# Kernel optimization log

Measured on AMD Instinct MI355X. Metric: run time of the kernel, lower is better.

Reference implementation:

```python
import jax, jax.numpy as jnp
import numpy as np

B, N, M, D, BD = 4, 128, 128, 256, 1024


def setup_inputs() -> dict:
    key = jax.random.key(0)
    k1, k2, k3, k4 = jax.random.split(key, 4)
    stdv = 1.0 / np.sqrt(D)
    X = jax.random.normal(k1, (B, N, D), dtype=jnp.float32)
    Y = jax.random.normal(k2, (B, M, D), dtype=jnp.float32)
    # bilinear tensor, init uniform(-stdv, stdv) as in reset_parameters
    A = jax.random.uniform(k3, (D, D, BD), minval=-stdv, maxval=stdv, dtype=jnp.float32)
    # final Linear(bd, 1)
    W = jax.random.uniform(k4, (1, BD), minval=-1.0 / np.sqrt(BD), maxval=1.0 / np.sqrt(BD), dtype=jnp.float32)
    b = jnp.zeros((1,), dtype=jnp.float32)
    return {"X": X, "Y": Y, "A": A, "W": W, "b": b}


def reference(X, Y, A, W, b):
    # Fused version of the per-slice loop: bi[b,n,m,k] = X[b,n,:] @ A[:,:,k] @ Y[b,m,:]
    # Step 1: contract X with A over d -> [B, N, d, bd]
    t = jnp.einsum('bnd,dek->bnek', X, A)
    # Step 2: contract with Y over the second feature dim -> [B, N, M, bd]
    bi = jnp.einsum('bnek,bme->bnmk', t, Y)
    # fc: single Linear(bd, 1), no trailing ReLU (fc_lst[:-1] drops it)
    S = jnp.einsum('bnmk,ok->bnmo', bi, W) + b
    return S[..., 0]  # squeeze to [B, N, M]
```

## Files before the change

kernel.cpp:

```cpp
#include <hip/hip_runtime.h>

#define DD   256
#define BD   1024
#define NB   4
#define NN   128
#define MM   128

__global__ __launch_bounds__(256) void reduce_A_kernel(
    const float* __restrict__ A, const float* __restrict__ W,
    float* __restrict__ Aw)
{
    __shared__ float wsh[BD];
    const int t = threadIdx.x;
#pragma unroll
    for (int i = 0; i < 4; ++i) wsh[t + i * 256] = W[t + i * 256];
    __syncthreads();

    const int lane = t & 63;
    const int wave = t >> 6;
    const long long row = (long long)blockIdx.x * 4 + wave;

    const float4* __restrict__ Arow = (const float4*)(A + row * BD);
    const float4* __restrict__ W4   = (const float4*)wsh;

    float acc = 0.f;
#pragma unroll
    for (int q = 0; q < 4; ++q) {
        float4 a = Arow[q * 64 + lane];
        float4 w = W4[q * 64 + lane];
        acc += a.x * w.x + a.y * w.y + a.z * w.z + a.w * w.w;
    }
#pragma unroll
    for (int off = 32; off > 0; off >>= 1)
        acc += __shfl_down(acc, off, 64);
    if (lane == 0) Aw[row] = acc;
}

__global__ __launch_bounds__(256) void bilinear_fused_kernel(
    const float* __restrict__ X, const float* __restrict__ Y,
    const float* __restrict__ Aw, const float* __restrict__ bias,
    float* __restrict__ S)
{
    const int bn = blockIdx.x;
    const int b  = bn >> 7;
    const int t  = threadIdx.x;

    __shared__ float xrow[DD];
    __shared__ float zrow[DD];
    __shared__ float partial[256];

    xrow[t] = X[(long long)bn * DD + t];
    __syncthreads();

    float acc = 0.f;
#pragma unroll 8
    for (int d = 0; d < DD; ++d) {
        acc += xrow[d] * Aw[d * DD + t];
    }
    zrow[t] = acc;
    __syncthreads();

    const int m  = t & 127;
    const int eh = (t >> 7) << 7;
    const float4* __restrict__ Y4 = (const float4*)(Y + ((long long)b * MM + m) * DD + eh);
    const float4* __restrict__ Z4 = (const float4*)(zrow + eh);

    float s = 0.f;
#pragma unroll 8
    for (int e = 0; e < 32; ++e) {
        float4 y = Y4[e];
        float4 z = Z4[e];
        s += z.x * y.x + z.y * y.y + z.z * y.z + z.w * y.w;
    }
    partial[t] = s;
    __syncthreads();

    if (t < 128) {
        S[(long long)bn * MM + t] = partial[t] + partial[t + 128] + bias[0];
    }
}

extern "C" void kernel_launch(void* const* d_in, const int* in_sizes, int n_in,
                              void* d_out, int out_size, void* d_ws, size_t ws_size,
                              hipStream_t stream) {
    const float* X    = (const float*)d_in[0];
    const float* Y    = (const float*)d_in[1];
    const float* A    = (const float*)d_in[2];
    const float* W    = (const float*)d_in[3];
    const float* bias = (const float*)d_in[4];
    float* S  = (float*)d_out;
    float* Aw = (float*)d_ws;

    reduce_A_kernel<<<dim3(65536 / 4), dim3(256), 0, stream>>>(A, W, Aw);

    bilinear_fused_kernel<<<dim3(NB * NN), dim3(256), 0, stream>>>(X, Y, Aw, bias, S);
}
```

Before: 376.5 us.

## Process four rows per wave in A-reduction and four X rows per block

The A·W reduction now has each wave handle four rows, with W held in registers instead of shared memory and A read through nontemporal loads; the four results go out as a single vector store. The bilinear kernel now gives each block four X rows, so every Aw and Y load is reused across four accumulators. This cuts the block count and the repeated Aw/Y traffic, at the cost of fewer blocks (128) in the second kernel and more register use.

```diff
diff --git a/kernel.cpp b/kernel.cpp
--- a/kernel.cpp
+++ b/kernel.cpp
@@ -6,34 +6,50 @@
 #define NN   128
 #define MM   128
 
+typedef float vfloat4 __attribute__((ext_vector_type(4)));
+
 __global__ __launch_bounds__(256) void reduce_A_kernel(
     const float* __restrict__ A, const float* __restrict__ W,
     float* __restrict__ Aw)
 {
-    __shared__ float wsh[BD];
-    const int t = threadIdx.x;
+    const int t    = threadIdx.x;
+    const int lane = t & 63;
+    const int wid  = t >> 6;
+    const int row0 = blockIdx.x * 16 + wid * 4;
+
+    const vfloat4* __restrict__ W4 = (const vfloat4*)W;
+    const vfloat4 w0 = W4[lane];
+    const vfloat4 w1 = W4[lane + 64];
+    const vfloat4 w2 = W4[lane + 128];
+    const vfloat4 w3 = W4[lane + 192];
+
+    const vfloat4* __restrict__ p = (const vfloat4*)(A + (size_t)row0 * BD) + lane;
+
+    float acc[4];
 #pragma unroll
-    for (int i = 0; i < 4; ++i) wsh[t + i * 256] = W[t + i * 256];
-    __syncthreads();
+    for (int r = 0; r < 4; ++r) {
+        const vfloat4* __restrict__ pr = p + r * 256;
+        vfloat4 a0 = __builtin_nontemporal_load(pr);
+        vfloat4 a1 = __builtin_nontemporal_load(pr + 64);
+        vfloat4 a2 = __builtin_nontemporal_load(pr + 128);
+        vfloat4 a3 = __builtin_nontemporal_load(pr + 192);
+        acc[r] = a0.x * w0.x + a0.y * w0.y + a0.z * w0.z + a0.w * w0.w
+               + a1.x * w1.x + a1.y * w1.y + a1.z * w1.z + a1.w * w1.w
+               + a2.x * w2.x + a2.y * w2.y + a2.z * w2.z + a2.w * w2.w
+               + a3.x * w3.x + a3.y * w3.y + a3.z * w3.z + a3.w * w3.w;
+    }
 
-    const int lane = t & 63;
-    const int wave = t >> 6;
-    const long long row = (long long)blockIdx.x * 4 + wave;
+#pragma unroll
+    for (int r = 0; r < 4; ++r) {
+#pragma unroll
+        for (int off = 32; off > 0; off >>= 1)
+            acc[r] += __shfl_down(acc[r], off, 64);
+    }
 
-    const float4* __restrict__ Arow = (const float4*)(A + row * BD);
-    const float4* __restrict__ W4   = (const float4*)wsh;
-
-    float acc = 0.f;
-#pragma unroll
-    for (int q = 0; q < 4; ++q) {
-        float4 a = Arow[q * 64 + lane];
-        float4 w = W4[q * 64 + lane];
-        acc += a.x * w.x + a.y * w.y + a.z * w.z + a.w * w.w;
+    if (lane == 0) {
+        vfloat4 out = {acc[0], acc[1], acc[2], acc[3]};
+        ((vfloat4*)Aw)[row0 >> 2] = out;
     }
-#pragma unroll
-    for (int off = 32; off > 0; off >>= 1)
-        acc += __shfl_down(acc, off, 64);
-    if (lane == 0) Aw[row] = acc;
 }
 
 __global__ __launch_bounds__(256) void bilinear_fused_kernel(
@@ -41,42 +57,57 @@
     const float* __restrict__ Aw, const float* __restrict__ bias,
     float* __restrict__ S)
 {
-    const int bn = blockIdx.x;
-    const int b  = bn >> 7;
-    const int t  = threadIdx.x;
+    const int bn0 = blockIdx.x * 4;
+    const int b   = bn0 >> 7;
+    const int t   = threadIdx.x;
 
-    __shared__ float xrow[DD];
-    __shared__ float zrow[DD];
-    __shared__ float partial[256];
+    __shared__ float xs[4][DD];
+    __shared__ float zs[4][DD];
+    __shared__ float partial[4][256];
 
-    xrow[t] = X[(long long)bn * DD + t];
+#pragma unroll
+    for (int r = 0; r < 4; ++r)
+        xs[r][t] = X[(size_t)(bn0 + r) * DD + t];
     __syncthreads();
 
-    float acc = 0.f;
-#pragma unroll 8
+    float acc0 = 0.f, acc1 = 0.f, acc2 = 0.f, acc3 = 0.f;
+#pragma unroll 4
     for (int d = 0; d < DD; ++d) {
-        acc += xrow[d] * Aw[d * DD + t];
+        float aw = Aw[d * DD + t];
+        acc0 += xs[0][d] * aw;
+        acc1 += xs[1][d] * aw;
+        acc2 += xs[2][d] * aw;
+        acc3 += xs[3][d] * aw;
     }
-    zrow[t] = acc;
+    zs[0][t] = acc0; zs[1][t] = acc1; zs[2][t] = acc2; zs[3][t] = acc3;
     __syncthreads();
 
     const int m  = t & 127;
     const int eh = (t >> 7) << 7;
-    const float4* __restrict__ Y4 = (const float4*)(Y + ((long long)b * MM + m) * DD + eh);
-    const float4* __restrict__ Z4 = (const float4*)(zrow + eh);
+    const float4* __restrict__ Y4 = (const float4*)(Y + ((size_t)b * MM + m) * DD + eh);
+    const float4* __restrict__ Z0 = (const float4*)(&zs[0][eh]);
+    const float4* __restrict__ Z1 = (const float4*)(&zs[1][eh]);
+    const float4* __restrict__ Z2 = (const float4*)(&zs[2][eh]);
+    const float4* __restrict__ Z3 = (const float4*)(&zs[3][eh]);
 
-    float s = 0.f;
+    float s0 = 0.f, s1 = 0.f, s2 = 0.f, s3 = 0.f;
 #pragma unroll 8
     for (int e = 0; e < 32; ++e) {
         float4 y = Y4[e];
-        float4 z = Z4[e];
-        s += z.x * y.x + z.y * y.y + z.z * y.z + z.w * y.w;
+        float4 z;
+        z = Z0[e]; s0 += z.x * y.x + z.y * y.y + z.z * y.z + z.w * y.w;
+        z = Z1[e]; s1 += z.x * y.x + z.y * y.y + z.z * y.z + z.w * y.w;
+        z = Z2[e]; s2 += z.x * y.x + z.y * y.y + z.z * y.z + z.w * y.w;
+        z = Z3[e]; s3 += z.x * y.x + z.y * y.y + z.z * y.z + z.w * y.w;
     }
-    partial[t] = s;
+    partial[0][t] = s0; partial[1][t] = s1; partial[2][t] = s2; partial[3][t] = s3;
     __syncthreads();
 
     if (t < 128) {
-        S[(long long)bn * MM + t] = partial[t] + partial[t + 128] + bias[0];
+        const float b0 = bias[0];
+#pragma unroll
+        for (int r = 0; r < 4; ++r)
+            S[(size_t)(bn0 + r) * MM + t] = partial[r][t] + partial[r][t + 128] + b0;
     }
 }
 
@@ -91,7 +122,6 @@
     float* S  = (float*)d_out;
     float* Aw = (float*)d_ws;
 
-    reduce_A_kernel<<<dim3(65536 / 4), dim3(256), 0, stream>>>(A, W, Aw);
-
-    bilinear_fused_kernel<<<dim3(NB * NN), dim3(256), 0, stream>>>(X, Y, Aw, bias, S);
+    reduce_A_kernel<<<dim3(65536 / 16), dim3(256), 0, stream>>>(A, W, Aw);
+    bilinear_fused_kernel<<<dim3(NB * NN / 4), dim3(256), 0, stream>>>(X, Y, Aw, bias, S);
 }
```

Result: faster. 361.8 us (-3.9%).
